# Optimization experiments

Hardware: AMD Instinct MI355X
Metric: run time of the kernel (lower is better)

The kernel has to match this reference:

```python
import jax, jax.numpy as jnp
import numpy as np

B, S, D_MODEL, D_INNER = 64, 128, 1024, 1024


def setup_inputs() -> dict:
    key = jax.random.key(0)
    ks = jax.random.split(key, 10)
    sc = 0.02
    return {
        "embeddings": jax.random.normal(ks[0], (B, S, D_MODEL), dtype=jnp.float32),
        "Wq": jax.random.normal(ks[1], (D_MODEL, D_INNER), dtype=jnp.float32) * sc,
        "bq": jnp.zeros((D_INNER,), dtype=jnp.float32),
        "Wk": jax.random.normal(ks[2], (D_MODEL, D_INNER), dtype=jnp.float32) * sc,
        "bk": jnp.zeros((D_INNER,), dtype=jnp.float32),
        "Wv": jax.random.normal(ks[3], (D_MODEL, D_INNER), dtype=jnp.float32) * sc,
        "bv": jnp.zeros((D_INNER,), dtype=jnp.float32),
        "w": jax.random.normal(ks[4], (S, S), dtype=jnp.float32) * sc,
        "Wo": jax.random.normal(ks[5], (D_INNER, D_MODEL), dtype=jnp.float32) * sc,
        "bo": jnp.zeros((D_MODEL,), dtype=jnp.float32),
    }


def reference(embeddings, Wq, bq, Wk, bk, Wv, bv, w, Wo, bo):
    # embeddings: [B, S, Dm]
    seq_len = embeddings.shape[1]
    q = embeddings @ Wq + bq          # [B, S, Di]
    k = embeddings @ Wk + bk
    v = embeddings @ Wv + bv

    max_k = jnp.max(k, axis=1, keepdims=True)   # [B, 1, Di]
    exp_k = jnp.exp(k - max_k)                  # [B, S, Di]

    max_w = jnp.max(w, axis=1, keepdims=True)   # [S, 1]
    wn = w - max_w                              # [S, S]
    tril = jnp.tril(jnp.ones((seq_len, seq_len), dtype=bool))
    wn = jnp.where(tril, wn[:seq_len, :seq_len], -jnp.inf)
    # torch.einsum('bjj,bjd->bjd', exp_w, x) picks the DIAGONAL of exp_w
    # (repeated subscript j) and multiplies elementwise along the seq dim.
    diag_w = jnp.exp(jnp.diagonal(wn))          # [S]; tril diagonal is True so finite
    dw = diag_w[None, :, None]                  # [1, S, 1]

    numerator = dw * (exp_k * v)                # [B, S, Di]
    denominator = dw * exp_k                    # [B, S, Di]
    out = jax.nn.sigmoid(q) * (numerator / denominator)
    return out @ Wo + bo                        # [B, S, Dm]
```

## Files before the change

kernel.cpp:

```cpp
#include <hip/hip_runtime.h>


typedef short bf16x8 __attribute__((ext_vector_type(8)));
typedef float f32x4  __attribute__((ext_vector_type(4)));

__device__ __forceinline__ short f2bf(float f) {
  union { float f; unsigned u; } x; x.f = f;
  unsigned r = x.u + 0x7fffu + ((x.u >> 16) & 1u);
  return (short)(r >> 16);
}

struct alignas(16) S8 { short v[8]; };

#define GLDS(g, l) \
  __builtin_amdgcn_global_load_lds((const __attribute__((address_space(1))) void*)(g), \
                                   (__attribute__((address_space(3))) void*)(l), 16, 0, 0)
#define BAR()    __builtin_amdgcn_s_barrier()
#define PRIO(x)  __builtin_amdgcn_s_setprio(x)
#define SCHED0() __builtin_amdgcn_sched_barrier(0)
#define VMCNT(N) asm volatile("s_waitcnt vmcnt(" #N ")" ::: "memory")
#define LGKM0()  asm volatile("s_waitcnt lgkmcnt(0)" ::: "memory")
#define MFMA(a, b, c) __builtin_amdgcn_mfma_f32_16x16x32_bf16((a), (b), (c), 0, 0, 0)

__global__ __launch_bounds__(256) void prep_kernel(
    const float* __restrict__ emb, const float* __restrict__ Wq, const float* __restrict__ Wv,
    const float* __restrict__ Wo, short* __restrict__ embB, short* __restrict__ WqvT,
    short* __restrict__ WoT) {
  __shared__ float tr[32 * 33];
  const int t = threadIdx.x;
  const int bid = blockIdx.x;
  const int gdim = gridDim.x;

  for (size_t i = (size_t)bid * 256 + t; i < 1048576; i += (size_t)gdim * 256) {
    const float4* p = (const float4*)emb + i * 2;
    float4 a = p[0], b = p[1];
    S8 s;
    s.v[0] = f2bf(a.x); s.v[1] = f2bf(a.y); s.v[2] = f2bf(a.z); s.v[3] = f2bf(a.w);
    s.v[4] = f2bf(b.x); s.v[5] = f2bf(b.y); s.v[6] = f2bf(b.z); s.v[7] = f2bf(b.w);
    ((S8*)embB)[i] = s;
  }

  int tx = t & 31, ty = t >> 5;
  for (int z = bid; z < 3072; z += gdim) {
    const float* in = (z < 1024) ? Wq : (z < 2048) ? Wv : Wo;
    short* op = (z < 1024) ? WqvT : (z < 2048) ? (WqvT + 1048576) : WoT;
    int ti = z & 1023;
    int bx = (ti & 31) * 32, by = (ti >> 5) * 32;
    __syncthreads();
#pragma unroll
    for (int i = 0; i < 32; i += 8)
      tr[(ty + i) * 33 + tx] = in[(size_t)(by + ty + i) * 1024 + bx + tx];
    __syncthreads();
#pragma unroll
    for (int i = 0; i < 32; i += 8)
      op[(size_t)(bx + ty + i) * 1024 + by + tx] = f2bf(tr[tx * 33 + ty + i]);
  }
}

__global__ __launch_bounds__(512, 2) void gemm_qv_kernel(
    const short* __restrict__ A, const short* __restrict__ BT,
    const float* __restrict__ bq, const float* __restrict__ bv, short* __restrict__ X) {
  __shared__ short As[2][256 * 64];
  __shared__ short Bqs[2][128 * 64];
  __shared__ short Bvs[2][128 * 64];
  const int t = threadIdx.x;
  const int lane = t & 63;
  const int w = t >> 6;
  const int l16 = lane & 15;
  const int quad = lane >> 4;
  const int b = blockIdx.x;
  const int wg = (b & 7) * 32 + (b >> 3);
  const int bm = (wg >> 3) * 256;
  const int bn = (wg & 7) * 128;
  const int wm = (w & 3) * 64;
  const int wn = (w >> 2) * 64;

  const int r8 = t >> 3;
  const int swe = ((t & 7) ^ (r8 & 7)) * 8;
  const short* gA = A + (size_t)(bm + r8) * 1024 + swe;
  const short* gq = BT + (size_t)(bn + r8) * 1024 + swe;
  const short* gv = BT + (size_t)(1024 + bn + r8) * 1024 + swe;
  short* lA = &As[0][0] + w * 512;
  short* lq = &Bqs[0][0] + w * 512;
  short* lv = &Bvs[0][0] + w * 512;

#define QV_STAGE(k, s) do {                                             \
    const short* a_ = gA + (k) * 64; short* la_ = lA + (s) * 16384;     \
    GLDS(a_, la_);               GLDS(a_ + 64 * 1024, la_ + 4096);      \
    GLDS(a_ + 128 * 1024, la_ + 8192); GLDS(a_ + 192 * 1024, la_ + 12288); \
    const short* q_ = gq + (k) * 64; short* lq_ = lq + (s) * 8192;      \
    GLDS(q_, lq_);               GLDS(q_ + 64 * 1024, lq_ + 4096);      \
    const short* v_ = gv + (k) * 64; short* lv_ = lv + (s) * 8192;      \
    GLDS(v_, lv_);               GLDS(v_ + 64 * 1024, lv_ + 4096);      \
  } while (0)

  const int csw0 = (quad ^ (l16 & 7)) * 8;
  const int csw1 = ((quad + 4) ^ (l16 & 7)) * 8;
  const short* fA0 = &As[0][0] + (wm + l16) * 64 + csw0;
  const short* fA1 = &As[0][0] + (wm + l16) * 64 + csw1;
  const short* fq0 = &Bqs[0][0] + (wn + l16) * 64 + csw0;
  const short* fq1 = &Bqs[0][0] + (wn + l16) * 64 + csw1;
  const short* fv0 = &Bvs[0][0] + (wn + l16) * 64 + csw0;
  const short* fv1 = &Bvs[0][0] + (wn + l16) * 64 + csw1;

  f32x4 aq[4][4] = {};
  f32x4 av[4][4] = {};

  QV_STAGE(0, 0);
  QV_STAGE(1, 1);

  for (int j = 0; j < 16; ++j) {
    const int s = j & 1;
    const short* sA0 = fA0 + s * 16384;
    const short* sA1 = fA1 + s * 16384;
    const short* sq0 = fq0 + s * 8192;
    const short* sq1 = fq1 + s * 8192;
    const short* sv0 = fv0 + s * 8192;
    const short* sv1 = fv1 + s * 8192;

    if (j < 15) { VMCNT(8); } else { VMCNT(0); }
    BAR();

    bf16x8 a0[4], a1[4], b0[2], b1[2];
#pragma unroll
    for (int i = 0; i < 4; ++i) {
      a0[i] = *(const bf16x8*)(sA0 + i * 1024);
      a1[i] = *(const bf16x8*)(sA1 + i * 1024);
    }
    b0[0] = *(const bf16x8*)(sq0);        b0[1] = *(const bf16x8*)(sq0 + 1024);
    b1[0] = *(const bf16x8*)(sq1);        b1[1] = *(const bf16x8*)(sq1 + 1024);
    BAR(); LGKM0(); SCHED0(); PRIO(1);
#pragma unroll
    for (int i = 0; i < 4; ++i)
#pragma unroll
      for (int n = 0; n < 2; ++n) {
        aq[i][n] = MFMA(a0[i], b0[n], aq[i][n]);
        aq[i][n] = MFMA(a1[i], b1[n], aq[i][n]);
      }
    PRIO(0); BAR();
    b0[0] = *(const bf16x8*)(sq0 + 2048);  b0[1] = *(const bf16x8*)(sq0 + 3072);
    b1[0] = *(const bf16x8*)(sq1 + 2048);  b1[1] = *(const bf16x8*)(sq1 + 3072);
    BAR(); LGKM0(); SCHED0(); PRIO(1);
#pragma unroll
    for (int i = 0; i < 4; ++i)
#pragma unroll
      for (int n = 0; n < 2; ++n) {
        aq[i][2 + n] = MFMA(a0[i], b0[n], aq[i][2 + n]);
        aq[i][2 + n] = MFMA(a1[i], b1[n], aq[i][2 + n]);
      }
    PRIO(0); BAR();
    b0[0] = *(const bf16x8*)(sv0);         b0[1] = *(const bf16x8*)(sv0 + 1024);
    b1[0] = *(const bf16x8*)(sv1);         b1[1] = *(const bf16x8*)(sv1 + 1024);
    BAR(); LGKM0(); SCHED0(); PRIO(1);
#pragma unroll
    for (int i = 0; i < 4; ++i)
#pragma unroll
      for (int n = 0; n < 2; ++n) {
        av[i][n] = MFMA(a0[i], b0[n], av[i][n]);
        av[i][n] = MFMA(a1[i], b1[n], av[i][n]);
      }
    PRIO(0); BAR();
    b0[0] = *(const bf16x8*)(sv0 + 2048);  b0[1] = *(const bf16x8*)(sv0 + 3072);
    b1[0] = *(const bf16x8*)(sv1 + 2048);  b1[1] = *(const bf16x8*)(sv1 + 3072);
    BAR(); LGKM0(); SCHED0(); PRIO(1);
#pragma unroll
    for (int i = 0; i < 4; ++i)
#pragma unroll
      for (int n = 0; n < 2; ++n) {
        av[i][2 + n] = MFMA(a0[i], b0[n], av[i][2 + n]);
        av[i][2 + n] = MFMA(a1[i], b1[n], av[i][2 + n]);
      }
    PRIO(0); BAR();
    if (j < 14) QV_STAGE(j + 2, s);
  }
#undef QV_STAGE

#pragma unroll
  for (int n = 0; n < 4; ++n) {
    const int col = bn + wn + n * 16 + l16;
    const float bql = bq[col], bvl = bv[col];
#pragma unroll
    for (int i = 0; i < 4; ++i)
#pragma unroll
      for (int r = 0; r < 4; ++r) {
        const int row = bm + wm + i * 16 + quad * 4 + r;
        const float q = aq[i][n][r] + bql;
        const float v = av[i][n][r] + bvl;
        const float sg = 1.0f / (1.0f + __expf(-q));
        X[(size_t)row * 1024 + col] = f2bf(sg * v);
      }
  }
}

__global__ __launch_bounds__(512, 2) void gemm_bt_kernel(
    const short* __restrict__ A, const short* __restrict__ BT, float* __restrict__ C,
    const float* __restrict__ bias) {
  __shared__ short As[2][256 * 64];
  __shared__ short Bs[2][128 * 64];
  const int t = threadIdx.x;
  const int lane = t & 63;
  const int w = t >> 6;
  const int l16 = lane & 15;
  const int quad = lane >> 4;
  const int b = blockIdx.x;
  const int wg = (b & 7) * 32 + (b >> 3);
  const int bm = (wg >> 3) * 256;
  const int bn = (wg & 7) * 128;
  const int wm = (w & 3) * 64;
  const int wn = (w >> 2) * 64;

  const int r8 = t >> 3;
  const int swe = ((t & 7) ^ (r8 & 7)) * 8;
  const short* gA = A + (size_t)(bm + r8) * 1024 + swe;
  const short* gB = BT + (size_t)(bn + r8) * 1024 + swe;
  short* lA = &As[0][0] + w * 512;
  short* lB = &Bs[0][0] + w * 512;

#define BT_STAGE(k, s) do {                                             \
    const short* a_ = gA + (k) * 64; short* la_ = lA + (s) * 16384;     \
    GLDS(a_, la_);               GLDS(a_ + 64 * 1024, la_ + 4096);      \
    GLDS(a_ + 128 * 1024, la_ + 8192); GLDS(a_ + 192 * 1024, la_ + 12288); \
    const short* b_ = gB + (k) * 64; short* lb_ = lB + (s) * 8192;      \
    GLDS(b_, lb_);               GLDS(b_ + 64 * 1024, lb_ + 4096);      \
  } while (0)

  const int csw0 = (quad ^ (l16 & 7)) * 8;
  const int csw1 = ((quad + 4) ^ (l16 & 7)) * 8;
  const short* fA0 = &As[0][0] + (wm + l16) * 64 + csw0;
  const short* fA1 = &As[0][0] + (wm + l16) * 64 + csw1;
  const short* fB0 = &Bs[0][0] + (wn + l16) * 64 + csw0;
  const short* fB1 = &Bs[0][0] + (wn + l16) * 64 + csw1;

  f32x4 acc[4][4] = {};

  BT_STAGE(0, 0);
  BT_STAGE(1, 1);

  for (int j = 0; j < 16; ++j) {
    const int s = j & 1;
    const short* sA0 = fA0 + s * 16384;
    const short* sA1 = fA1 + s * 16384;
    const short* sB0 = fB0 + s * 8192;
    const short* sB1 = fB1 + s * 8192;

    if (j < 15) { VMCNT(6); } else { VMCNT(0); }
    BAR();

    bf16x8 a0[4], a1[4], b0[2], b1[2];
#pragma unroll
    for (int i = 0; i < 4; ++i) {
      a0[i] = *(const bf16x8*)(sA0 + i * 1024);
      a1[i] = *(const bf16x8*)(sA1 + i * 1024);
    }
    b0[0] = *(const bf16x8*)(sB0);        b0[1] = *(const bf16x8*)(sB0 + 1024);
    b1[0] = *(const bf16x8*)(sB1);        b1[1] = *(const bf16x8*)(sB1 + 1024);
    BAR(); LGKM0(); SCHED0(); PRIO(1);
#pragma unroll
    for (int i = 0; i < 4; ++i)
#pragma unroll
      for (int n = 0; n < 2; ++n) {
        acc[i][n] = MFMA(a0[i], b0[n], acc[i][n]);
        acc[i][n] = MFMA(a1[i], b1[n], acc[i][n]);
      }
    PRIO(0); BAR();
    b0[0] = *(const bf16x8*)(sB0 + 2048);  b0[1] = *(const bf16x8*)(sB0 + 3072);
    b1[0] = *(const bf16x8*)(sB1 + 2048);  b1[1] = *(const bf16x8*)(sB1 + 3072);
    BAR(); LGKM0(); SCHED0(); PRIO(1);
#pragma unroll
    for (int i = 0; i < 4; ++i)
#pragma unroll
      for (int n = 0; n < 2; ++n) {
        acc[i][2 + n] = MFMA(a0[i], b0[n], acc[i][2 + n]);
        acc[i][2 + n] = MFMA(a1[i], b1[n], acc[i][2 + n]);
      }
    PRIO(0); BAR();
    if (j < 14) BT_STAGE(j + 2, s);
  }
#undef BT_STAGE

#pragma unroll
  for (int n = 0; n < 4; ++n) {
    const int col = bn + wn + n * 16 + l16;
    const float bl = bias[col];
#pragma unroll
    for (int i = 0; i < 4; ++i)
#pragma unroll
      for (int r = 0; r < 4; ++r) {
        const int row = bm + wm + i * 16 + quad * 4 + r;
        C[(size_t)row * 1024 + col] = acc[i][n][r] + bl;
      }
  }
}

extern "C" void kernel_launch(void* const* d_in, const int* in_sizes, int n_in,
                              void* d_out, int out_size, void* d_ws, size_t ws_size,
                              hipStream_t stream) {
  const float* emb = (const float*)d_in[0];
  const float* Wq  = (const float*)d_in[1];
  const float* bq  = (const float*)d_in[2];
  const float* Wv  = (const float*)d_in[5];
  const float* bv  = (const float*)d_in[6];
  const float* Wo  = (const float*)d_in[8];
  const float* bo  = (const float*)d_in[9];
  float* out = (float*)d_out;

  char* ws = (char*)d_ws;
  short* embB = (short*)(ws);
  short* X    = (short*)(ws + 16777216);
  short* WqvT = (short*)(ws + 33554432);
  short* WoT  = (short*)(ws + 37748736);

  prep_kernel<<<1024, 256, 0, stream>>>(emb, Wq, Wv, Wo, embB, WqvT, WoT);
  gemm_qv_kernel<<<256, 512, 0, stream>>>(embB, WqvT, bq, bv, X);
  gemm_bt_kernel<<<256, 512, 0, stream>>>(X, WoT, out, bo);
}
```

Before: 173.9 us.

## Interleave global-to-LDS prefetch with MFMA phases and widen weight transpose tiles

Both GEMM main loops are reorganised so that each phase loads the full B fragments for one K-half and the next stage's global_load_lds prefetches are issued between MFMA groups, instead of all at the end of the iteration. The goal is to overlap memory traffic with compute and cut the number of LDS read phases. The weight transpose in the prep kernel moves to 64x64 tiles with float4 reads and 16-byte bf16 writes, and the prep grid shrinks to 256 blocks. Issuing prefetches into the stage buffer while other waves may still be reading from it depends on barrier placement, which raises ordering risk.

New measurement: 167.7 us. -3.6%, faster.

```diff
diff --git a/kernel.cpp b/kernel.cpp
--- a/kernel.cpp
+++ b/kernel.cpp
@@ -26,7 +26,7 @@
     const float* __restrict__ emb, const float* __restrict__ Wq, const float* __restrict__ Wv,
     const float* __restrict__ Wo, short* __restrict__ embB, short* __restrict__ WqvT,
     short* __restrict__ WoT) {
-  __shared__ float tr[32 * 33];
+  __shared__ float tr[64 * 65];
   const int t = threadIdx.x;
   const int bid = blockIdx.x;
   const int gdim = gridDim.x;
@@ -40,20 +40,30 @@
     ((S8*)embB)[i] = s;
   }
 
-  int tx = t & 31, ty = t >> 5;
-  for (int z = bid; z < 3072; z += gdim) {
-    const float* in = (z < 1024) ? Wq : (z < 2048) ? Wv : Wo;
-    short* op = (z < 1024) ? WqvT : (z < 2048) ? (WqvT + 1048576) : WoT;
-    int ti = z & 1023;
-    int bx = (ti & 31) * 32, by = (ti >> 5) * 32;
+  const int rr = t >> 4, cc4 = (t & 15) * 4;
+  const int orow = t >> 3, ocol8 = (t & 7) * 8;
+  for (int z = bid; z < 768; z += gdim) {
+    const float* in; short* op; int ti;
+    if (z < 256)      { in = Wq; op = WqvT;           ti = z; }
+    else if (z < 512) { in = Wv; op = WqvT + 1048576; ti = z - 256; }
+    else              { in = Wo; op = WoT;            ti = z - 512; }
+    const int bx = (ti & 15) * 64, by = (ti >> 4) * 64;
     __syncthreads();
 #pragma unroll
-    for (int i = 0; i < 32; i += 8)
-      tr[(ty + i) * 33 + tx] = in[(size_t)(by + ty + i) * 1024 + bx + tx];
+    for (int k = 0; k < 4; ++k) {
+      float4 v = *(const float4*)&in[(size_t)(by + rr + 16 * k) * 1024 + bx + cc4];
+      float* d = &tr[(rr + 16 * k) * 65 + cc4];
+      d[0] = v.x; d[1] = v.y; d[2] = v.z; d[3] = v.w;
+    }
     __syncthreads();
 #pragma unroll
-    for (int i = 0; i < 32; i += 8)
-      op[(size_t)(bx + ty + i) * 1024 + by + tx] = f2bf(tr[tx * 33 + ty + i]);
+    for (int h = 0; h < 2; ++h) {
+      const int oc = orow + 32 * h;
+      S8 s;
+#pragma unroll
+      for (int i = 0; i < 8; ++i) s.v[i] = f2bf(tr[(ocol8 + i) * 65 + oc]);
+      *(S8*)&op[(size_t)(bx + oc) * 1024 + by + ocol8] = s;
+    }
   }
 }
 
@@ -121,57 +131,58 @@
     if (j < 15) { VMCNT(8); } else { VMCNT(0); }
     BAR();
 
-    bf16x8 a0[4], a1[4], b0[2], b1[2];
+    bf16x8 a0[4], a1[4], bq0[4], bq1[4], bv0[4], bv1[4];
 #pragma unroll
     for (int i = 0; i < 4; ++i) {
       a0[i] = *(const bf16x8*)(sA0 + i * 1024);
       a1[i] = *(const bf16x8*)(sA1 + i * 1024);
-    }
-    b0[0] = *(const bf16x8*)(sq0);        b0[1] = *(const bf16x8*)(sq0 + 1024);
-    b1[0] = *(const bf16x8*)(sq1);        b1[1] = *(const bf16x8*)(sq1 + 1024);
+      bq0[i] = *(const bf16x8*)(sq0 + i * 1024);
+    }
     BAR(); LGKM0(); SCHED0(); PRIO(1);
 #pragma unroll
     for (int i = 0; i < 4; ++i)
 #pragma unroll
-      for (int n = 0; n < 2; ++n) {
-        aq[i][n] = MFMA(a0[i], b0[n], aq[i][n]);
-        aq[i][n] = MFMA(a1[i], b1[n], aq[i][n]);
-      }
-    PRIO(0); BAR();
-    b0[0] = *(const bf16x8*)(sq0 + 2048);  b0[1] = *(const bf16x8*)(sq0 + 3072);
-    b1[0] = *(const bf16x8*)(sq1 + 2048);  b1[1] = *(const bf16x8*)(sq1 + 3072);
+      for (int n = 0; n < 4; ++n)
+        aq[i][n] = MFMA(a0[i], bq0[n], aq[i][n]);
+    PRIO(0); BAR();
+#pragma unroll
+    for (int i = 0; i < 4; ++i) {
+      bq1[i] = *(const bf16x8*)(sq1 + i * 1024);
+      bv0[i] = *(const bf16x8*)(sv0 + i * 1024);
+      bv1[i] = *(const bf16x8*)(sv1 + i * 1024);
+    }
     BAR(); LGKM0(); SCHED0(); PRIO(1);
 #pragma unroll
     for (int i = 0; i < 4; ++i)
 #pragma unroll
-      for (int n = 0; n < 2; ++n) {
-        aq[i][2 + n] = MFMA(a0[i], b0[n], aq[i][2 + n]);
-        aq[i][2 + n] = MFMA(a1[i], b1[n], aq[i][2 + n]);
-      }
-    PRIO(0); BAR();
-    b0[0] = *(const bf16x8*)(sv0);         b0[1] = *(const bf16x8*)(sv0 + 1024);
-    b1[0] = *(const bf16x8*)(sv1);         b1[1] = *(const bf16x8*)(sv1 + 1024);
-    BAR(); LGKM0(); SCHED0(); PRIO(1);
-#pragma unroll
-    for (int i = 0; i < 4; ++i)
-#pragma unroll
-      for (int n = 0; n < 2; ++n) {
-        av[i][n] = MFMA(a0[i], b0[n], av[i][n]);
-        av[i][n] = MFMA(a1[i], b1[n], av[i][n]);
-      }
-    PRIO(0); BAR();
-    b0[0] = *(const bf16x8*)(sv0 + 2048);  b0[1] = *(const bf16x8*)(sv0 + 3072);
-    b1[0] = *(const bf16x8*)(sv1 + 2048);  b1[1] = *(const bf16x8*)(sv1 + 3072);
-    BAR(); LGKM0(); SCHED0(); PRIO(1);
-#pragma unroll
-    for (int i = 0; i < 4; ++i)
-#pragma unroll
-      for (int n = 0; n < 2; ++n) {
-        av[i][2 + n] = MFMA(a0[i], b0[n], av[i][2 + n]);
-        av[i][2 + n] = MFMA(a1[i], b1[n], av[i][2 + n]);
-      }
-    PRIO(0); BAR();
-    if (j < 14) QV_STAGE(j + 2, s);
+      for (int n = 0; n < 4; ++n)
+        aq[i][n] = MFMA(a1[i], bq1[n], aq[i][n]);
+    PRIO(0); BAR();
+    if (j < 14) {
+      const short* a_ = gA + (j + 2) * 64; short* la_ = lA + s * 16384;
+      GLDS(a_, la_);                     GLDS(a_ + 64 * 1024, la_ + 4096);
+      GLDS(a_ + 128 * 1024, la_ + 8192); GLDS(a_ + 192 * 1024, la_ + 12288);
+    }
+    PRIO(1);
+#pragma unroll
+    for (int i = 0; i < 4; ++i)
+#pragma unroll
+      for (int n = 0; n < 4; ++n)
+        av[i][n] = MFMA(a0[i], bv0[n], av[i][n]);
+    PRIO(0); BAR();
+    if (j < 14) {
+      const short* q_ = gq + (j + 2) * 64; short* lq_ = lq + s * 8192;
+      GLDS(q_, lq_); GLDS(q_ + 64 * 1024, lq_ + 4096);
+      const short* v_ = gv + (j + 2) * 64; short* lv_ = lv + s * 8192;
+      GLDS(v_, lv_); GLDS(v_ + 64 * 1024, lv_ + 4096);
+    }
+    PRIO(1);
+#pragma unroll
+    for (int i = 0; i < 4; ++i)
+#pragma unroll
+      for (int n = 0; n < 4; ++n)
+        av[i][n] = MFMA(a1[i], bv1[n], av[i][n]);
+    PRIO(0); BAR();
   }
 #undef QV_STAGE
 
@@ -246,35 +257,54 @@
     if (j < 15) { VMCNT(6); } else { VMCNT(0); }
     BAR();
 
-    bf16x8 a0[4], a1[4], b0[2], b1[2];
+    bf16x8 a0[4], a1[4], b0[4], b1[4];
 #pragma unroll
     for (int i = 0; i < 4; ++i) {
       a0[i] = *(const bf16x8*)(sA0 + i * 1024);
       a1[i] = *(const bf16x8*)(sA1 + i * 1024);
-    }
-    b0[0] = *(const bf16x8*)(sB0);        b0[1] = *(const bf16x8*)(sB0 + 1024);
-    b1[0] = *(const bf16x8*)(sB1);        b1[1] = *(const bf16x8*)(sB1 + 1024);
+      b0[i] = *(const bf16x8*)(sB0 + i * 1024);
+    }
     BAR(); LGKM0(); SCHED0(); PRIO(1);
 #pragma unroll
     for (int i = 0; i < 4; ++i)
 #pragma unroll
-      for (int n = 0; n < 2; ++n) {
+      for (int n = 0; n < 2; ++n)
         acc[i][n] = MFMA(a0[i], b0[n], acc[i][n]);
+    PRIO(0); BAR();
+#pragma unroll
+    for (int i = 0; i < 4; ++i) b1[i] = *(const bf16x8*)(sB1 + i * 1024);
+    BAR(); LGKM0(); SCHED0(); PRIO(1);
+#pragma unroll
+    for (int i = 0; i < 4; ++i)
+#pragma unroll
+      for (int n = 0; n < 2; ++n)
+        acc[i][2 + n] = MFMA(a0[i], b0[2 + n], acc[i][2 + n]);
+    PRIO(0); BAR();
+    if (j < 14) {
+      const short* a_ = gA + (j + 2) * 64; short* la_ = lA + s * 16384;
+      GLDS(a_, la_); GLDS(a_ + 64 * 1024, la_ + 4096);
+      GLDS(a_ + 128 * 1024, la_ + 8192);
+    }
+    PRIO(1);
+#pragma unroll
+    for (int i = 0; i < 4; ++i)
+#pragma unroll
+      for (int n = 0; n < 2; ++n)
         acc[i][n] = MFMA(a1[i], b1[n], acc[i][n]);
-      }
-    PRIO(0); BAR();
-    b0[0] = *(const bf16x8*)(sB0 + 2048);  b0[1] = *(const bf16x8*)(sB0 + 3072);
-    b1[0] = *(const bf16x8*)(sB1 + 2048);  b1[1] = *(const bf16x8*)(sB1 + 3072);
-    BAR(); LGKM0(); SCHED0(); PRIO(1);
-#pragma unroll
-    for (int i = 0; i < 4; ++i)
-#pragma unroll
-      for (int n = 0; n < 2; ++n) {
-        acc[i][2 + n] = MFMA(a0[i], b0[n], acc[i][2 + n]);
-        acc[i][2 + n] = MFMA(a1[i], b1[n], acc[i][2 + n]);
-      }
-    PRIO(0); BAR();
-    if (j < 14) BT_STAGE(j + 2, s);
+    PRIO(0); BAR();
+    if (j < 14) {
+      const short* a_ = gA + (j + 2) * 64; short* la_ = lA + s * 16384;
+      GLDS(a_ + 192 * 1024, la_ + 12288);
+      const short* b_ = gB + (j + 2) * 64; short* lb_ = lB + s * 8192;
+      GLDS(b_, lb_); GLDS(b_ + 64 * 1024, lb_ + 4096);
+    }
+    PRIO(1);
+#pragma unroll
+    for (int i = 0; i < 4; ++i)
+#pragma unroll
+      for (int n = 0; n < 2; ++n)
+        acc[i][2 + n] = MFMA(a1[i], b1[2 + n], acc[i][2 + n]);
+    PRIO(0); BAR();
   }
 #undef BT_STAGE
 
@@ -310,7 +340,7 @@
   short* WqvT = (short*)(ws + 33554432);
   short* WoT  = (short*)(ws + 37748736);
 
-  prep_kernel<<<1024, 256, 0, stream>>>(emb, Wq, Wv, Wo, embB, WqvT, WoT);
+  prep_kernel<<<256, 256, 0, stream>>>(emb, Wq, Wv, Wo, embB, WqvT, WoT);
   gemm_qv_kernel<<<256, 512, 0, stream>>>(embB, WqvT, bq, bv, X);
   gemm_bt_kernel<<<256, 512, 0, stream>>>(X, WoT, out, bo);
 }
```
